# Optimization experiments

Hardware: AMD Instinct MI355X
Metric: run time of the kernel (lower is better)

Reference implementation:

```python
import jax, jax.numpy as jnp
import numpy as np

N_QUBITS = 12
N_LAYERS = 6
BATCH = 512

def _apply_1q(state, U, wire):
    # state: (B, 2, ..., 2); U: (2,2) shared across batch or (B,2,2) batched
    ax = wire + 1
    s = jnp.moveaxis(state, ax, -1)
    if U.ndim == 3:
        s = jnp.einsum('bij,b...j->b...i', U, s)
    else:
        s = jnp.einsum('ij,b...j->b...i', U, s)
    return jnp.moveaxis(s, -1, ax)

def _apply_cnot(state, ctrl, tgt):
    ca, ta = ctrl + 1, tgt + 1
    s0 = jnp.take(state, 0, axis=ca)
    s1 = jnp.take(state, 1, axis=ca)
    ta2 = ta - 1 if ta > ca else ta  # axis shift after removing ctrl axis
    s1 = jnp.flip(s1, axis=ta2)      # X on target where control == 1
    return jnp.stack([s0, s1], axis=ca)

def _rot_matrix(phi, theta, omega):
    # PennyLane Rot = RZ(omega) @ RY(theta) @ RZ(phi)
    c = jnp.cos(theta / 2)
    s = jnp.sin(theta / 2)
    a = jnp.exp(-0.5j * (phi + omega)) * c
    b = -jnp.exp(0.5j * (phi - omega)) * s
    cc = jnp.exp(-0.5j * (phi - omega)) * s
    d = jnp.exp(0.5j * (phi + omega)) * c
    return jnp.stack([jnp.stack([a, b]), jnp.stack([cc, d])]).astype(jnp.complex64)

def _layer(state, w):
    # w: (N_QUBITS, 3) -> per-wire Rot, then CNOT ring
    for j in range(N_QUBITS):
        state = _apply_1q(state, _rot_matrix(w[j, 0], w[j, 1], w[j, 2]), j)
    for j in range(N_QUBITS):
        state = _apply_cnot(state, j, (j + 1) % N_QUBITS)
    return state

def _circuit(feats, weights):
    B = feats.shape[0]
    state = jnp.zeros((B,) + (2,) * N_QUBITS, jnp.complex64)
    state = state.at[(slice(None),) + (0,) * N_QUBITS].set(1.0)  # |0...0>
    # AngleEmbedding rotation='X': batched RX(feats[:, j]) on wire j
    for j in range(N_QUBITS):
        half = feats[:, j] / 2
        c = jnp.cos(half).astype(jnp.complex64)
        m = (-1j) * jnp.sin(half).astype(jnp.complex64)
        U = jnp.stack([jnp.stack([c, m], -1), jnp.stack([m, c], -1)], -2)  # (B,2,2)
        state = _apply_1q(state, U, j)
    lay = jax.checkpoint(_layer)
    for i in range(N_LAYERS):
        state = lay(state, weights[i])
    # <Z_0>: marginal probability on wire 0
    probs = jnp.sum(jnp.abs(state) ** 2, axis=tuple(range(2, N_QUBITS + 1)))  # (B, 2)
    return probs[:, 0] - probs[:, 1]

def setup_inputs():
    key = jax.random.key(0)
    k1, k2 = jax.random.split(key)
    x = jax.random.normal(k1, (BATCH, 3, 224, 224), jnp.float32)
    weights = jax.random.uniform(k2, (N_LAYERS, N_QUBITS, 3), jnp.float32, 0.0, 2.0 * np.pi)
    bias = jnp.zeros((), jnp.float32)
    return {"x": x, "weights": weights, "bias": bias}

def reference(x, weights, bias):
    B = x.shape[0]
    feats = x.reshape(B, -1)[:, :N_QUBITS]
    q_out = _circuit(feats, weights)
    return (q_out + bias)[:, None]  # (B, 1)
```

## Files before the change

### kernel.cpp

```cpp
#include <hip/hip_runtime.h>

#define NLAYERS 6
#define XROW 150528


__global__ void qnn_prep(const float* __restrict__ w, float* __restrict__ coef) {
    const int g = threadIdx.x;
    if (g < NLAYERS * 12) {
        const float phi = w[g*3+0], th = w[g*3+1], om = w[g*3+2];
        const float ct = cosf(0.5f*th), st = sinf(0.5f*th);
        const float sp = 0.5f*(phi+om), dm = 0.5f*(phi-om);
        const float csp = cosf(sp), ssp = sinf(sp);
        const float cdm = cosf(dm), sdm = sinf(dm);
        float* c = coef + g*8;
        c[0] =  csp*ct; c[1] = -ssp*ct;
        c[2] = -cdm*st; c[3] = -sdm*st;
        c[4] =  cdm*st; c[5] = -sdm*st;
        c[6] =  csp*ct; c[7] =  ssp*ct;
    }
}

template<int BP>
__device__ __forceinline__ void rot_local(float (&vr)[16], float (&vi)[16],
                                          const float* __restrict__ cf) {
    const float ar = cf[0], ai = cf[1], br = cf[2], bi = cf[3];
    const float cr = cf[4], ci = cf[5], dr = cf[6], di = cf[7];
    #pragma unroll
    for (int l0 = 0; l0 < 16; ++l0) {
        if (!(l0 & (1 << BP))) {
            const int l1 = l0 | (1 << BP);
            const float r0 = vr[l0], i0 = vi[l0];
            const float r1 = vr[l1], i1 = vi[l1];
            vr[l0] = ar*r0 - ai*i0 + br*r1 - bi*i1;
            vi[l0] = ar*i0 + ai*r0 + br*i1 + bi*r1;
            vr[l1] = cr*r0 - ci*i0 + dr*r1 - di*i1;
            vi[l1] = cr*i0 + ci*r0 + dr*i1 + di*r1;
        }
    }
}

#define SWAP_AMP(A,B) { float t_ = vr[A]; vr[A] = vr[B]; vr[B] = t_; \
                        t_ = vi[A]; vi[A] = vi[B]; vi[B] = t_; }
#define RING_CNOTS_LOCAL() \
    SWAP_AMP(8,12) SWAP_AMP(9,13) SWAP_AMP(10,14) SWAP_AMP(11,15) \
    SWAP_AMP(4,6)  SWAP_AMP(5,7)  SWAP_AMP(12,14) SWAP_AMP(13,15) \
    SWAP_AMP(2,3)  SWAP_AMP(6,7)  SWAP_AMP(10,11) SWAP_AMP(14,15)

__global__ __launch_bounds__(256, 2) void qnn_kernel(
    const float* __restrict__ x,
    const float* __restrict__ coef,
    const float* __restrict__ bias,
    float* __restrict__ out)
{
    __shared__ float2 st[4096];
    __shared__ float partial[4];

    const int tid  = threadIdx.x;
    const int lane = tid & 63;
    const int wv   = tid >> 6;
    const int b    = blockIdx.x;

    float vr[16], vi[16];

    const float* xb = x + (size_t)b * XROW;
    float fc[12], fs[12];
    #pragma unroll
    for (int j = 0; j < 12; ++j) {
        const float h = xb[j] * 0.5f;
        fc[j] = __cosf(h);
        fs[j] = __sinf(h);
    }
    float pr = 1.f, pi_ = 0.f;
    #pragma unroll
    for (int j = 4; j < 12; ++j) {
        const int bit = (j < 10) ? ((lane >> (9 - j)) & 1)
                                 : ((j == 10) ? ((wv >> 1) & 1) : (wv & 1));
        const float nr = bit ? (pi_ * fs[j]) : (pr * fc[j]);
        const float ni = bit ? (-pr * fs[j]) : (pi_ * fc[j]);
        pr = nr; pi_ = ni;
    }
    vr[0] = pr; vi[0] = pi_;
    #pragma unroll
    for (int bb = 0; bb < 4; ++bb) {
        const int wire = 3 - bb;
        const float cc = fc[wire], ss = fs[wire];
        const int m = 1 << bb;
        #pragma unroll
        for (int l = 0; l < 8; ++l) {
            if (l < m) {
                const float r = vr[l], q = vi[l];
                vr[l + m] = q * ss;
                vi[l + m] = -r * ss;
                vr[l] = r * cc;
                vi[l] = q * cc;
            }
        }
    }

    for (int layer = 0; layer < NLAYERS; ++layer) {
        const float* cl = coef + layer * 12 * 8;

        if (layer) {
            #pragma unroll
            for (int l = 0; l < 16; ++l)
                st[(l << 8) | (tid ^ l ^ wv)] = make_float2(vr[l], vi[l]);
            __syncthreads();
            {
                const int l_old = ((lane & 3) << 2) | wv;
                const int w_old = (lane >> 2) & 3;
                const int n_lo  = (lane >> 4) & 3;
                const int fold  = (wv & 1) << 3;
                #pragma unroll
                for (int l = 0; l < 16; ++l) {
                    const int lp2   = l ^ fold;
                    const int n_old = (lp2 << 2) | n_lo;
                    const int t_old = (w_old << 6) | n_old;
                    const float2 v  = st[(l_old << 8) | (t_old ^ l_old ^ w_old)];
                    vr[l] = v.x; vi[l] = v.y;
                }
            }
            __syncthreads();
        }

        rot_local<3>(vr, vi, cl + 0*8);
        rot_local<2>(vr, vi, cl + 1*8);
        rot_local<1>(vr, vi, cl + 2*8);
        rot_local<0>(vr, vi, cl + 3*8);
        RING_CNOTS_LOCAL();

        #pragma unroll
        for (int l = 0; l < 16; ++l)
            st[(l << 8) | (tid ^ (l << 2))] = make_float2(vr[l], vi[l]);
        __syncthreads();
        {
            const int l_old = (lane >> 2) & 0xF;
            const int n_lo  = lane & 3;
            #pragma unroll
            for (int l = 0; l < 16; ++l) {
                const int n_old = (l << 2) | n_lo;
                const int t_old = (wv << 6) | n_old;
                const float2 v  = st[(l_old << 8) | (t_old ^ (l_old << 2))];
                vr[l] = v.x; vi[l] = v.y;
            }
        }
        __syncthreads();

        rot_local<3>(vr, vi, cl + 4*8);
        rot_local<2>(vr, vi, cl + 5*8);
        rot_local<1>(vr, vi, cl + 6*8);
        rot_local<0>(vr, vi, cl + 7*8);
        {
            const bool sel = (lane >> 2) & 1;
            #pragma unroll
            for (int l = 0; l < 8; ++l) {
                const float a0 = vr[l], a1 = vr[l + 8];
                vr[l] = sel ? a1 : a0;  vr[l + 8] = sel ? a0 : a1;
                const float b0 = vi[l], b1 = vi[l + 8];
                vi[l] = sel ? b1 : b0;  vi[l + 8] = sel ? b0 : b1;
            }
        }
        RING_CNOTS_LOCAL();

        #pragma unroll
        for (int l = 0; l < 16; ++l) {
            const int sw = ((l & 1) << 3) | ((l & 2) << 1) | ((l & 4) >> 1) | ((l & 8) >> 3);
            st[(l << 8) | (tid ^ sw)] = make_float2(vr[l], vi[l]);
        }
        __syncthreads();
        {
            const int l_old = ((lane & 3) << 2) | wv;
            const int swo = ((l_old & 1) << 3) | ((l_old & 2) << 1)
                          | ((l_old & 4) >> 1) | ((l_old & 8) >> 3);
            const int n_hi = ((lane >> 2) & 0xF) << 2;
            #pragma unroll
            for (int l = 0; l < 16; ++l) {
                const int n_old = n_hi | (l >> 2);
                const int w_old = l & 3;
                const int t_old = (w_old << 6) | n_old;
                const float2 v  = st[(l_old << 8) | (t_old ^ swo)];
                vr[l] = v.x; vi[l] = v.y;
            }
        }
        __syncthreads();

        rot_local<3>(vr, vi, cl + 8*8);
        rot_local<2>(vr, vi, cl + 9*8);
        rot_local<1>(vr, vi, cl + 10*8);
        rot_local<0>(vr, vi, cl + 11*8);
        {
            const bool sel = wv & 1;
            #pragma unroll
            for (int l = 0; l < 8; ++l) {
                const float a0 = vr[l], a1 = vr[l + 8];
                vr[l] = sel ? a1 : a0;  vr[l + 8] = sel ? a0 : a1;
                const float b0 = vi[l], b1 = vi[l + 8];
                vi[l] = sel ? b1 : b0;  vi[l + 8] = sel ? b0 : b1;
            }
        }
        RING_CNOTS_LOCAL();
    }

    float acc = 0.f;
    #pragma unroll
    for (int l = 0; l < 16; ++l) {
        const float p = vr[l] * vr[l] + vi[l] * vi[l];
        acc += ((((lane >> 5) ^ l) & 1) ? -p : p);
    }
    #pragma unroll
    for (int off = 32; off > 0; off >>= 1)
        acc += __shfl_down(acc, off, 64);
    if ((lane) == 0) partial[wv] = acc;
    __syncthreads();
    if (tid == 0)
        out[b] = partial[0] + partial[1] + partial[2] + partial[3] + bias[0];
}

extern "C" void kernel_launch(void* const* d_in, const int* in_sizes, int n_in,
                              void* d_out, int out_size, void* d_ws, size_t ws_size,
                              hipStream_t stream) {
    const float* x    = (const float*)d_in[0];
    const float* wts  = (const float*)d_in[1];
    const float* bias = (const float*)d_in[2];
    float* out  = (float*)d_out;
    float* coef = (float*)d_ws;
    qnn_prep<<<1, 128, 0, stream>>>(wts, coef);
    qnn_kernel<<<out_size, 256, 0, stream>>>(x, coef, bias, out);
}
```

Before: 382.5 us.

## Pack amplitudes as float2 vectors and double-buffer shared memory to drop barriers

Amplitudes are now held as two-wide float vectors, and the complex 2x2 rotation uses packed FMAs so the compiler can emit packed fp32 instructions. The shared-memory transpose buffer is double-buffered, which removes the second __syncthreads after each exchange; a write to one buffer cannot race with reads of the other. The cost is twice the LDS per block (64 KB instead of 32 KB), which may limit occupancy. Packed math also adds lane shuffles to build the swapped (-imag, real) vectors.

```diff
diff --git a/kernel.cpp b/kernel.cpp
--- a/kernel.cpp
+++ b/kernel.cpp
@@ -2,6 +2,8 @@
 
 #define NLAYERS 6
 #define XROW 150528
+
+typedef float v2f __attribute__((ext_vector_type(2)));
 
 
 __global__ void qnn_prep(const float* __restrict__ w, float* __restrict__ coef) {
@@ -20,27 +22,30 @@
     }
 }
 
+__device__ __forceinline__ v2f cfma(float s, v2f a, v2f c) {
+    v2f sv = {s, s};
+    return __builtin_elementwise_fma(sv, a, c);
+}
+
 template<int BP>
-__device__ __forceinline__ void rot_local(float (&vr)[16], float (&vi)[16],
-                                          const float* __restrict__ cf) {
+__device__ __forceinline__ void rot_local(v2f (&v)[16], const float* __restrict__ cf) {
     const float ar = cf[0], ai = cf[1], br = cf[2], bi = cf[3];
     const float cr = cf[4], ci = cf[5], dr = cf[6], di = cf[7];
     #pragma unroll
     for (int l0 = 0; l0 < 16; ++l0) {
         if (!(l0 & (1 << BP))) {
             const int l1 = l0 | (1 << BP);
-            const float r0 = vr[l0], i0 = vi[l0];
-            const float r1 = vr[l1], i1 = vi[l1];
-            vr[l0] = ar*r0 - ai*i0 + br*r1 - bi*i1;
-            vi[l0] = ar*i0 + ai*r0 + br*i1 + bi*r1;
-            vr[l1] = cr*r0 - ci*i0 + dr*r1 - di*i1;
-            vi[l1] = cr*i0 + ci*r0 + dr*i1 + di*r1;
-        }
-    }
-}
-
-#define SWAP_AMP(A,B) { float t_ = vr[A]; vr[A] = vr[B]; vr[B] = t_; \
-                        t_ = vi[A]; vi[A] = vi[B]; vi[B] = t_; }
+            const v2f u0 = v[l0], u1 = v[l1];
+            const v2f t0 = {-u0.y, u0.x};
+            const v2f t1 = {-u1.y, u1.x};
+            const v2f sar = {ar, ar}, scr = {cr, cr};
+            v[l0] = cfma(bi, t1, cfma(br, u1, cfma(ai, t0, sar * u0)));
+            v[l1] = cfma(di, t1, cfma(dr, u1, cfma(ci, t0, scr * u0)));
+        }
+    }
+}
+
+#define SWAP_AMP(A,B) { v2f t_ = v[A]; v[A] = v[B]; v[B] = t_; }
 #define RING_CNOTS_LOCAL() \
     SWAP_AMP(8,12) SWAP_AMP(9,13) SWAP_AMP(10,14) SWAP_AMP(11,15) \
     SWAP_AMP(4,6)  SWAP_AMP(5,7)  SWAP_AMP(12,14) SWAP_AMP(13,15) \
@@ -52,7 +57,7 @@
     const float* __restrict__ bias,
     float* __restrict__ out)
 {
-    __shared__ float2 st[4096];
+    __shared__ v2f st[2][4096];
     __shared__ float partial[4];
 
     const int tid  = threadIdx.x;
@@ -60,7 +65,8 @@
     const int wv   = tid >> 6;
     const int b    = blockIdx.x;
 
-    float vr[16], vi[16];
+    v2f v[16];
+    int pb = 0;
 
     const float* xb = x + (size_t)b * XROW;
     float fc[12], fs[12];
@@ -79,7 +85,7 @@
         const float ni = bit ? (-pr * fs[j]) : (pi_ * fc[j]);
         pr = nr; pi_ = ni;
     }
-    vr[0] = pr; vi[0] = pi_;
+    v[0] = (v2f){pr, pi_};
     #pragma unroll
     for (int bb = 0; bb < 4; ++bb) {
         const int wire = 3 - bb;
@@ -88,22 +94,21 @@
         #pragma unroll
         for (int l = 0; l < 8; ++l) {
             if (l < m) {
-                const float r = vr[l], q = vi[l];
-                vr[l + m] = q * ss;
-                vi[l + m] = -r * ss;
-                vr[l] = r * cc;
-                vi[l] = q * cc;
+                const float r = v[l].x, q = v[l].y;
+                v[l + m] = (v2f){q * ss, -r * ss};
+                v[l]     = (v2f){r * cc,  q * cc};
             }
         }
     }
 
     for (int layer = 0; layer < NLAYERS; ++layer) {
-        const float* cl = coef + layer * 12 * 8;
+        const float* cl = coef + layer * 96;
 
         if (layer) {
+            v2f* S = st[pb];
             #pragma unroll
             for (int l = 0; l < 16; ++l)
-                st[(l << 8) | (tid ^ l ^ wv)] = make_float2(vr[l], vi[l]);
+                S[(l << 8) | (tid ^ l ^ wv)] = v[l];
             __syncthreads();
             {
                 const int l_old = ((lane & 3) << 2) | wv;
@@ -115,59 +120,58 @@
                     const int lp2   = l ^ fold;
                     const int n_old = (lp2 << 2) | n_lo;
                     const int t_old = (w_old << 6) | n_old;
-                    const float2 v  = st[(l_old << 8) | (t_old ^ l_old ^ w_old)];
-                    vr[l] = v.x; vi[l] = v.y;
+                    v[l] = S[(l_old << 8) | (t_old ^ l_old ^ w_old)];
                 }
             }
+            pb ^= 1;
+        }
+
+        rot_local<3>(v, cl + 0*8);
+        rot_local<2>(v, cl + 1*8);
+        rot_local<1>(v, cl + 2*8);
+        rot_local<0>(v, cl + 3*8);
+        RING_CNOTS_LOCAL();
+
+        {
+            v2f* S = st[pb];
+            #pragma unroll
+            for (int l = 0; l < 16; ++l)
+                S[(l << 8) | (tid ^ (l << 2))] = v[l];
             __syncthreads();
-        }
-
-        rot_local<3>(vr, vi, cl + 0*8);
-        rot_local<2>(vr, vi, cl + 1*8);
-        rot_local<1>(vr, vi, cl + 2*8);
-        rot_local<0>(vr, vi, cl + 3*8);
-        RING_CNOTS_LOCAL();
-
-        #pragma unroll
-        for (int l = 0; l < 16; ++l)
-            st[(l << 8) | (tid ^ (l << 2))] = make_float2(vr[l], vi[l]);
-        __syncthreads();
-        {
             const int l_old = (lane >> 2) & 0xF;
             const int n_lo  = lane & 3;
             #pragma unroll
             for (int l = 0; l < 16; ++l) {
                 const int n_old = (l << 2) | n_lo;
                 const int t_old = (wv << 6) | n_old;
-                const float2 v  = st[(l_old << 8) | (t_old ^ (l_old << 2))];
-                vr[l] = v.x; vi[l] = v.y;
-            }
-        }
-        __syncthreads();
-
-        rot_local<3>(vr, vi, cl + 4*8);
-        rot_local<2>(vr, vi, cl + 5*8);
-        rot_local<1>(vr, vi, cl + 6*8);
-        rot_local<0>(vr, vi, cl + 7*8);
+                v[l] = S[(l_old << 8) | (t_old ^ (l_old << 2))];
+            }
+            pb ^= 1;
+        }
+
+        rot_local<3>(v, cl + 4*8);
+        rot_local<2>(v, cl + 5*8);
+        rot_local<1>(v, cl + 6*8);
+        rot_local<0>(v, cl + 7*8);
         {
             const bool sel = (lane >> 2) & 1;
             #pragma unroll
             for (int l = 0; l < 8; ++l) {
-                const float a0 = vr[l], a1 = vr[l + 8];
-                vr[l] = sel ? a1 : a0;  vr[l + 8] = sel ? a0 : a1;
-                const float b0 = vi[l], b1 = vi[l + 8];
-                vi[l] = sel ? b1 : b0;  vi[l + 8] = sel ? b0 : b1;
+                const v2f a0 = v[l], a1 = v[l + 8];
+                v[l]     = sel ? a1 : a0;
+                v[l + 8] = sel ? a0 : a1;
             }
         }
         RING_CNOTS_LOCAL();
 
-        #pragma unroll
-        for (int l = 0; l < 16; ++l) {
-            const int sw = ((l & 1) << 3) | ((l & 2) << 1) | ((l & 4) >> 1) | ((l & 8) >> 3);
-            st[(l << 8) | (tid ^ sw)] = make_float2(vr[l], vi[l]);
-        }
-        __syncthreads();
-        {
+        {
+            v2f* S = st[pb];
+            #pragma unroll
+            for (int l = 0; l < 16; ++l) {
+                const int sw = ((l & 1) << 3) | ((l & 2) << 1) | ((l & 4) >> 1) | ((l & 8) >> 3);
+                S[(l << 8) | (tid ^ sw)] = v[l];
+            }
+            __syncthreads();
             const int l_old = ((lane & 3) << 2) | wv;
             const int swo = ((l_old & 1) << 3) | ((l_old & 2) << 1)
                           | ((l_old & 4) >> 1) | ((l_old & 8) >> 3);
@@ -177,24 +181,22 @@
                 const int n_old = n_hi | (l >> 2);
                 const int w_old = l & 3;
                 const int t_old = (w_old << 6) | n_old;
-                const float2 v  = st[(l_old << 8) | (t_old ^ swo)];
-                vr[l] = v.x; vi[l] = v.y;
-            }
-        }
-        __syncthreads();
-
-        rot_local<3>(vr, vi, cl + 8*8);
-        rot_local<2>(vr, vi, cl + 9*8);
-        rot_local<1>(vr, vi, cl + 10*8);
-        rot_local<0>(vr, vi, cl + 11*8);
+                v[l] = S[(l_old << 8) | (t_old ^ swo)];
+            }
+            pb ^= 1;
+        }
+
+        rot_local<3>(v, cl + 8*8);
+        rot_local<2>(v, cl + 9*8);
+        rot_local<1>(v, cl + 10*8);
+        rot_local<0>(v, cl + 11*8);
         {
             const bool sel = wv & 1;
             #pragma unroll
             for (int l = 0; l < 8; ++l) {
-                const float a0 = vr[l], a1 = vr[l + 8];
-                vr[l] = sel ? a1 : a0;  vr[l + 8] = sel ? a0 : a1;
-                const float b0 = vi[l], b1 = vi[l + 8];
-                vi[l] = sel ? b1 : b0;  vi[l + 8] = sel ? b0 : b1;
+                const v2f a0 = v[l], a1 = v[l + 8];
+                v[l]     = sel ? a1 : a0;
+                v[l + 8] = sel ? a0 : a1;
             }
         }
         RING_CNOTS_LOCAL();
@@ -203,13 +205,13 @@
     float acc = 0.f;
     #pragma unroll
     for (int l = 0; l < 16; ++l) {
-        const float p = vr[l] * vr[l] + vi[l] * vi[l];
+        const float p = v[l].x * v[l].x + v[l].y * v[l].y;
         acc += ((((lane >> 5) ^ l) & 1) ? -p : p);
     }
     #pragma unroll
     for (int off = 32; off > 0; off >>= 1)
         acc += __shfl_down(acc, off, 64);
-    if ((lane) == 0) partial[wv] = acc;
+    if (lane == 0) partial[wv] = acc;
     __syncthreads();
     if (tid == 0)
         out[b] = partial[0] + partial[1] + partial[2] + partial[3] + bias[0];
```

Result: faster. 371.3 us (-2.9%).
